# Kernel tuning notes

Hardware: AMD Instinct MI355X
Metric: run time of the kernel (lower is better)

## Reference

```python
import jax, jax.numpy as jnp
import numpy as np

NUM_STEPS = 100
STEP = 2.0 / (NUM_STEPS - 1)          # bin width over [-1, 1]
EPS = 1.0 / NUM_STEPS
TSIZE = NUM_STEPS                      # bin centers t_k = -1 + k*STEP, k=0..99
B, D = 4096, 128
NUM_CLASSES = 100


def setup_inputs() -> dict:
    key = jax.random.key(0)
    k1, k2 = jax.random.split(key)
    embeddings = jax.random.normal(k1, (B, D), dtype=jnp.float32)
    classes = jax.random.randint(k2, (B,), 0, NUM_CLASSES)
    return {"embeddings": embeddings, "classes": classes}


def _histogram_loss(embeddings, classes):
    n = embeddings.shape[0]
    iu, ju = np.triu_indices(n, 1)            # static upper-triangular pair indices
    # cosine similarity of all pairs (outer_cosine_similarity)
    en = embeddings / jnp.linalg.norm(embeddings, axis=1, keepdims=True)
    dists = en @ en.T                          # [B, B]
    s = jnp.clip(dists[iu, ju], -1.0 + 1e-6, 1.0 - 1e-6)   # [P]
    pos = (classes[iu] == classes[ju])         # [P] bool

    # soft triangular-kernel 2-bin scatter (equivalent to indsa/indsb masking):
    # bin j gets (t_j + STEP - s)/STEP, bin j+1 gets (s - t_j)/STEP
    j = jnp.floor((s + 1.0 - 1e-6) / STEP).astype(jnp.int32)   # lower bin index
    t_j = j.astype(s.dtype) * STEP - 1.0
    w_hi = (s - t_j) / STEP                    # weight for bin j+1
    w_lo = (t_j + STEP - s) / STEP             # weight for bin j

    def histogram(mask):
        m = mask.astype(s.dtype)
        size = m.sum()
        h = jnp.zeros((TSIZE,), dtype=s.dtype)
        h = h.at[j].add(w_lo * m).at[j + 1].add(w_hi * m)
        return h / size

    hist_pos = histogram(pos)
    hist_neg = histogram(~pos)
    # tril-masked repeat + sum(0) in the original is exactly a cumulative sum
    hist_pos_cdf = jnp.cumsum(hist_pos)
    return jnp.sum(hist_neg * hist_pos_cdf)


def reference(embeddings, classes):
    return _histogram_loss(embeddings, classes)
```

## Files before the change

### kernel.cpp

```cpp
#include <hip/hip_runtime.h>
#include <hip/hip_bf16.h>
#include <cstddef>

#define BN 4096
#define DD 128
#define NSTEPS 100
#define PTILE 128
#define PLSTR 136
#define GRID_T (BN / PTILE)
#define NOFF 496
#define NBLK 528
#define NREPC 16

typedef __attribute__((ext_vector_type(8))) short bf16x8;
typedef __attribute__((ext_vector_type(4))) float f32x4;

__device__ __forceinline__ void faddf(float* p, float v) { unsafeAtomicAdd(p, v); }

__global__ __launch_bounds__(256) void hl_normalize(const float* __restrict__ emb,
                                                    ushort* __restrict__ out) {
    int w = threadIdx.x >> 6;
    int lane = threadIdx.x & 63;
    int row = (blockIdx.x << 2) + w;
    const float2 v = *(const float2*)(emb + (size_t)row * DD + 2 * lane);
    float ss = v.x * v.x + v.y * v.y;
    #pragma unroll
    for (int off = 32; off > 0; off >>= 1) ss += __shfl_xor(ss, off);
    float inv = 1.0f / sqrtf(ss);
    __hip_bfloat16 b0 = __float2bfloat16(v.x * inv);
    __hip_bfloat16 b1 = __float2bfloat16(v.y * inv);
    ushort2 pk;
    pk.x = *(ushort*)&b0;
    pk.y = *(ushort*)&b1;
    *(ushort2*)(out + (size_t)row * DD + 2 * lane) = pk;
}

__global__ __launch_bounds__(256) void hl_poscls(const ushort* __restrict__ nemb,
                                                 const int* __restrict__ cls,
                                                 float* __restrict__ gPos) {
    const int c = blockIdx.x;
    __shared__ int idx[256];
    __shared__ int scan[256];
    __shared__ ushort As[64 * PLSTR];
    __shared__ ushort Bs[64 * PLSTR];
    __shared__ float hpos[NREPC * 101];
    __shared__ int mTot;
    const int tid = threadIdx.x;

    for (int i = tid; i < NREPC * 101; i += 256) hpos[i] = 0.f;

    const int base = tid * 16;
    int myCnt = 0;
    #pragma unroll
    for (int k = 0; k < 16; ++k) myCnt += (cls[base + k] == c);
    scan[tid] = myCnt;
    __syncthreads();
    for (int s = 1; s < 256; s <<= 1) {
        int v = (tid >= s) ? scan[tid - s] : 0;
        __syncthreads();
        scan[tid] += v;
        __syncthreads();
    }
    int w = scan[tid] - myCnt;
    if (tid == 255) mTot = scan[255] > 256 ? 256 : scan[255];
    #pragma unroll
    for (int k = 0; k < 16; ++k) {
        if (cls[base + k] == c && w < 256) { idx[w] = base + k; ++w; }
    }
    __syncthreads();
    const int m = mTot;
    const int nt = (m + 63) >> 6;

    constexpr float STEPF = 2.0f / 99.0f;
    constexpr float INVSTEP = 49.5f;
    constexpr float CLIPV = 1.0f - 1e-6f;

    const int lane = tid & 63;
    const int wv = tid >> 6;
    const int lr = lane & 15;
    const int kg = lane >> 4;
    const int rep = (lane & 15) * 101;

    for (int si = 0; si < nt; ++si) {
        for (int sj = si; sj < nt; ++sj) {
            __syncthreads();
            #pragma unroll
            for (int it = 0; it < 4; ++it) {
                int q = it * 256 + tid;
                int row = q >> 4;
                int ch = q & 15;
                int ga = si * 64 + row;
                int gb = sj * 64 + row;
                int ra = idx[ga < m ? ga : 0];
                int rb = idx[gb < m ? gb : 0];
                *(float4*)(&As[row * PLSTR + ch * 8]) =
                    *(const float4*)(nemb + (size_t)ra * DD + ch * 8);
                *(float4*)(&Bs[row * PLSTR + ch * 8]) =
                    *(const float4*)(nemb + (size_t)rb * DD + ch * 8);
            }
            __syncthreads();

            f32x4 zero4 = {0.f, 0.f, 0.f, 0.f};
            f32x4 pacc[4] = {zero4, zero4, zero4, zero4};
            #pragma unroll
            for (int ks = 0; ks < 4; ++ks) {
                bf16x8 af = *(const bf16x8*)(&As[(wv * 16 + lr) * PLSTR + ks * 32 + kg * 8]);
                #pragma unroll
                for (int fb = 0; fb < 4; ++fb) {
                    bf16x8 bf = *(const bf16x8*)(&Bs[(fb * 16 + lr) * PLSTR + ks * 32 + kg * 8]);
                    pacc[fb] = __builtin_amdgcn_mfma_f32_16x16x32_bf16(af, bf, pacc[fb], 0, 0, 0);
                }
            }

            #pragma unroll
            for (int fb = 0; fb < 4; ++fb) {
                const int gb = sj * 64 + fb * 16 + lr;
                #pragma unroll
                for (int j = 0; j < 4; ++j) {
                    const int ga = si * 64 + wv * 16 + kg * 4 + j;
                    if (ga < gb && gb < m) {
                        float s = pacc[fb][j];
                        s = fminf(fmaxf(s, -CLIPV), CLIPV);
                        float u = (s + CLIPV) * INVSTEP;
                        int jb = (int)u;
                        if (jb > 98) jb = 98;
                        float t_j = (float)jb * STEPF - 1.0f;
                        float w_hi = (s - t_j) * INVSTEP;
                        float w_lo = 1.0f - w_hi;
                        faddf(&hpos[rep + jb], w_lo);
                        faddf(&hpos[rep + jb + 1], w_hi);
                    }
                }
            }
        }
    }
    __syncthreads();
    if (tid < NSTEPS) {
        float v = 0.f;
        #pragma unroll
        for (int r = 0; r < NREPC; ++r) v += hpos[r * 101 + tid];
        if (v != 0.f) faddf(&gPos[tid], v);
    }
}

__global__ __launch_bounds__(256, 2) void hl_neg(const ushort* __restrict__ nemb,
                                                 const int* __restrict__ cls,
                                                 const float* __restrict__ gPos,
                                                 float* __restrict__ gLoss,
                                                 float* __restrict__ gCnt,
                                                 unsigned int* __restrict__ gDone,
                                                 float* __restrict__ out) {
    int ti, tj;
    {
        int t = blockIdx.x;
        if (t < NOFF) {
            ti = 0;
            int rem = t;
            while (rem >= GRID_T - 1 - ti) { rem -= GRID_T - 1 - ti; ++ti; }
            tj = ti + 1 + rem;
        } else {
            ti = tj = t - NOFF;
        }
    }

    __shared__ ushort As[PTILE * PLSTR];
    __shared__ ushort Bs[PTILE * PLSTR];
    __shared__ float cdfL[NREPC * 101];
    __shared__ float scan[128];
    __shared__ float red[9];
    __shared__ int clsA[PTILE], clsB[PTILE];

    const int tid = threadIdx.x;
    if (tid < PTILE) clsA[tid] = cls[ti * PTILE + tid];
    else             clsB[tid - PTILE] = cls[tj * PTILE + (tid - PTILE)];

    if (tid < 128) scan[tid] = (tid < NSTEPS) ? gPos[tid] : 0.f;
    __syncthreads();
    for (int off = 1; off < 128; off <<= 1) {
        float v = 0.f;
        if (tid < 128 && tid >= off) v = scan[tid - off];
        __syncthreads();
        if (tid < 128) scan[tid] += v;
        __syncthreads();
    }
    if (tid == 0) red[8] = scan[NSTEPS - 1];
    __syncthreads();
    const float invsp = 1.0f / red[8];
    for (int i = tid; i < NREPC * NSTEPS; i += 256) {
        int r = i / NSTEPS, b = i - r * NSTEPS;
        cdfL[r * 101 + b] = scan[b] * invsp;
    }

    #pragma unroll
    for (int it = 0; it < 8; ++it) {
        int idx = it * 256 + tid;
        int row = idx >> 4;
        int cch = idx & 15;
        const float4 va = *(const float4*)(nemb + (size_t)(ti * PTILE + row) * DD + cch * 8);
        const float4 vb = *(const float4*)(nemb + (size_t)(tj * PTILE + row) * DD + cch * 8);
        *(float4*)(&As[row * PLSTR + cch * 8]) = va;
        *(float4*)(&Bs[row * PLSTR + cch * 8]) = vb;
    }
    __syncthreads();

    const int lane = tid & 63;
    const int wid = tid >> 6;
    const int wr = wid >> 1, wc = wid & 1;
    const int lr = lane & 15;
    const int kg = lane >> 4;

    f32x4 zero4 = {0.f, 0.f, 0.f, 0.f};
    f32x4 acc[4][4];
    #pragma unroll
    for (int a = 0; a < 4; ++a)
        #pragma unroll
        for (int b = 0; b < 4; ++b) acc[a][b] = zero4;

    #pragma unroll
    for (int ks = 0; ks < 4; ++ks) {
        bf16x8 af[4], bfr[4];
        #pragma unroll
        for (int f = 0; f < 4; ++f) {
            int arow = wr * 64 + f * 16 + lr;
            af[f] = *(const bf16x8*)(&As[arow * PLSTR + ks * 32 + kg * 8]);
            int brow = wc * 64 + f * 16 + lr;
            bfr[f] = *(const bf16x8*)(&Bs[brow * PLSTR + ks * 32 + kg * 8]);
        }
        #pragma unroll
        for (int fa = 0; fa < 4; ++fa)
            #pragma unroll
            for (int fb = 0; fb < 4; ++fb)
                acc[fa][fb] = __builtin_amdgcn_mfma_f32_16x16x32_bf16(af[fa], bfr[fb], acc[fa][fb], 0, 0, 0);
    }

    constexpr float STEPF = 2.0f / 99.0f;
    constexpr float INVSTEP = 49.5f;
    constexpr float CLIPV = 1.0f - 1e-6f;

    const int li_base = wr * 64 + (kg << 2);
    const int lj_base = wc * 64 + lr;
    const float* crep = &cdfL[(lane & 15) * 101];

    int ca[16];
    #pragma unroll
    for (int fa = 0; fa < 4; ++fa)
        #pragma unroll
        for (int j = 0; j < 4; ++j) ca[fa * 4 + j] = clsA[li_base + fa * 16 + j];

    const bool offdiag = (ti != tj);
    float lacc = 0.f, lcnt = 0.f;

    #pragma unroll
    for (int fb = 0; fb < 4; ++fb) {
        const int lj = lj_base + fb * 16;
        const int cb = clsB[lj];
        #pragma unroll
        for (int fa = 0; fa < 4; ++fa) {
            const int li0 = li_base + fa * 16;
            f32x4 v = acc[fa][fb];
            #pragma unroll
            for (int j = 0; j < 4; ++j) {
                const int li = li0 + j;
                const bool mneg = (offdiag || (li < lj)) && (ca[fa * 4 + j] != cb);
                float s = v[j];
                s = fminf(fmaxf(s, -CLIPV), CLIPV);
                float u = (s + CLIPV) * INVSTEP;
                int jb = (int)u;
                if (jb > 98) jb = 98;
                float t_j = (float)jb * STEPF - 1.0f;
                float w_hi = (s - t_j) * INVSTEP;
                float w_lo = 1.0f - w_hi;
                float c0 = crep[jb];
                float c1 = crep[jb + 1];
                float m = mneg ? 1.0f : 0.0f;
                lacc = fmaf(m, fmaf(w_lo, c0, w_hi * c1), lacc);
                lcnt += m;
            }
        }
    }

    #pragma unroll
    for (int off = 32; off > 0; off >>= 1) {
        lacc += __shfl_xor(lacc, off);
        lcnt += __shfl_xor(lcnt, off);
    }
    if (lane == 0) { red[wid] = lacc; red[4 + wid] = lcnt; }
    __syncthreads();
    if (tid == 0) {
        float L = red[0] + red[1] + red[2] + red[3];
        float C = red[4] + red[5] + red[6] + red[7];
        faddf(&gLoss[blockIdx.x & 31], L);
        faddf(&gCnt[blockIdx.x & 31], C);
        __threadfence();
        unsigned int tk = atomicAdd(gDone, 1u);
        if (tk == NBLK - 1) {
            __threadfence();
            float ls = 0.f, cs = 0.f;
            for (int i = 0; i < 32; ++i) {
                ls += __hip_atomic_load(&gLoss[i], __ATOMIC_RELAXED, __HIP_MEMORY_SCOPE_AGENT);
                cs += __hip_atomic_load(&gCnt[i], __ATOMIC_RELAXED, __HIP_MEMORY_SCOPE_AGENT);
            }
            out[0] = ls / cs;
        }
    }
}

extern "C" void kernel_launch(void* const* d_in, const int* in_sizes, int n_in,
                              void* d_out, int out_size, void* d_ws, size_t ws_size,
                              hipStream_t stream) {
    const float* emb = (const float*)d_in[0];
    const int* classes = (const int*)d_in[1];
    float* out = (float*)d_out;

    ushort* nemb = (ushort*)d_ws;
    float* gPos = (float*)((char*)d_ws + (size_t)BN * DD * sizeof(ushort));
    float* gLoss = gPos + NSTEPS;
    float* gCnt = gLoss + 32;
    unsigned int* gDone = (unsigned int*)(gCnt + 32);

    hipMemsetAsync(gPos, 0, (NSTEPS + 64 + 1) * sizeof(float), stream);

    hl_normalize<<<BN / 4, 256, 0, stream>>>(emb, nemb);
    hl_poscls<<<NSTEPS, 256, 0, stream>>>(nemb, classes, gPos);
    hl_neg<<<NBLK, 256, 0, stream>>>(nemb, classes, gPos, gLoss, gCnt, gDone, out);
}
```

Baseline: 47.03 us.

## Fold memset into normalize, precompute CDF once, use direct-to-LDS swizzled loads

Removes the hipMemsetAsync by zeroing the control block inside the normalize kernel. The last poscls block, chosen with an atomic counter, computes the normalized positive CDF once, so each neg block no longer runs its own prefix scan. The neg kernel packs two diagonal tiles per block, which cuts the grid from 528 to 512 blocks, and diagonal tiles reuse the A tile as B. Tile loads go through global_load_lds into an XOR-swizzled unpadded LDS layout, replacing the padded register-staged copies. The trade-offs are extra serial work in the last poscls block and a longer run for the blocks that handle two diagonal tiles.

```diff
diff --git a/kernel.cpp b/kernel.cpp
--- a/kernel.cpp
+++ b/kernel.cpp
@@ -9,7 +9,7 @@
 #define PLSTR 136
 #define GRID_T (BN / PTILE)
 #define NOFF 496
-#define NBLK 528
+#define NBLK2 512
 #define NREPC 16
 
 typedef __attribute__((ext_vector_type(8))) short bf16x8;
@@ -17,8 +17,12 @@
 
 __device__ __forceinline__ void faddf(float* p, float v) { unsafeAtomicAdd(p, v); }
 
+#define ZERON 166
+
 __global__ __launch_bounds__(256) void hl_normalize(const float* __restrict__ emb,
-                                                    ushort* __restrict__ out) {
+                                                    ushort* __restrict__ out,
+                                                    float* __restrict__ zero_blk) {
+    if (blockIdx.x == 0 && threadIdx.x < ZERON) zero_blk[threadIdx.x] = 0.f;
     int w = threadIdx.x >> 6;
     int lane = threadIdx.x & 63;
     int row = (blockIdx.x << 2) + w;
@@ -37,7 +41,9 @@
 
 __global__ __launch_bounds__(256) void hl_poscls(const ushort* __restrict__ nemb,
                                                  const int* __restrict__ cls,
-                                                 float* __restrict__ gPos) {
+                                                 float* __restrict__ gPos,
+                                                 unsigned int* __restrict__ gDoneP,
+                                                 float* __restrict__ gCdf) {
     const int c = blockIdx.x;
     __shared__ int idx[256];
     __shared__ int scan[256];
@@ -45,6 +51,7 @@
     __shared__ ushort Bs[64 * PLSTR];
     __shared__ float hpos[NREPC * 101];
     __shared__ int mTot;
+    __shared__ int lastFlag;
     const int tid = threadIdx.x;
 
     for (int i = tid; i < NREPC * 101; i += 256) hpos[i] = 0.f;
@@ -141,140 +148,177 @@
         for (int r = 0; r < NREPC; ++r) v += hpos[r * 101 + tid];
         if (v != 0.f) faddf(&gPos[tid], v);
     }
+    __threadfence();
+    if (tid == 0) {
+        unsigned int tk = atomicAdd(gDoneP, 1u);
+        lastFlag = (tk == NSTEPS - 1);
+    }
+    __syncthreads();
+    if (lastFlag) {
+        float v = (tid < NSTEPS)
+            ? __hip_atomic_load(&gPos[tid], __ATOMIC_RELAXED, __HIP_MEMORY_SCOPE_AGENT) : 0.f;
+        if (tid < 128) hpos[tid] = v;
+        __syncthreads();
+        for (int off = 1; off < 128; off <<= 1) {
+            float x = 0.f;
+            if (tid < 128 && tid >= off) x = hpos[tid - off];
+            __syncthreads();
+            if (tid < 128) hpos[tid] += x;
+            __syncthreads();
+        }
+        const float invsp = 1.0f / hpos[NSTEPS - 1];
+        if (tid < NSTEPS) gCdf[tid] = hpos[tid] * invsp;
+    }
 }
 
 __global__ __launch_bounds__(256, 2) void hl_neg(const ushort* __restrict__ nemb,
                                                  const int* __restrict__ cls,
-                                                 const float* __restrict__ gPos,
+                                                 const float* __restrict__ gCdf,
                                                  float* __restrict__ gLoss,
                                                  float* __restrict__ gCnt,
                                                  unsigned int* __restrict__ gDone,
                                                  float* __restrict__ out) {
-    int ti, tj;
-    {
-        int t = blockIdx.x;
-        if (t < NOFF) {
-            ti = 0;
-            int rem = t;
-            while (rem >= GRID_T - 1 - ti) { rem -= GRID_T - 1 - ti; ++ti; }
-            tj = ti + 1 + rem;
-        } else {
-            ti = tj = t - NOFF;
-        }
-    }
-
-    __shared__ ushort As[PTILE * PLSTR];
-    __shared__ ushort Bs[PTILE * PLSTR];
+    __shared__ ushort As[PTILE * 128];
+    __shared__ ushort Bs[PTILE * 128];
     __shared__ float cdfL[NREPC * 101];
-    __shared__ float scan[128];
-    __shared__ float red[9];
+    __shared__ float red[8];
     __shared__ int clsA[PTILE], clsB[PTILE];
 
     const int tid = threadIdx.x;
-    if (tid < PTILE) clsA[tid] = cls[ti * PTILE + tid];
-    else             clsB[tid - PTILE] = cls[tj * PTILE + (tid - PTILE)];
-
-    if (tid < 128) scan[tid] = (tid < NSTEPS) ? gPos[tid] : 0.f;
-    __syncthreads();
-    for (int off = 1; off < 128; off <<= 1) {
-        float v = 0.f;
-        if (tid < 128 && tid >= off) v = scan[tid - off];
-        __syncthreads();
-        if (tid < 128) scan[tid] += v;
-        __syncthreads();
-    }
-    if (tid == 0) red[8] = scan[NSTEPS - 1];
-    __syncthreads();
-    const float invsp = 1.0f / red[8];
-    for (int i = tid; i < NREPC * NSTEPS; i += 256) {
-        int r = i / NSTEPS, b = i - r * NSTEPS;
-        cdfL[r * 101 + b] = scan[b] * invsp;
-    }
-
-    #pragma unroll
-    for (int it = 0; it < 8; ++it) {
-        int idx = it * 256 + tid;
-        int row = idx >> 4;
-        int cch = idx & 15;
-        const float4 va = *(const float4*)(nemb + (size_t)(ti * PTILE + row) * DD + cch * 8);
-        const float4 vb = *(const float4*)(nemb + (size_t)(tj * PTILE + row) * DD + cch * 8);
-        *(float4*)(&As[row * PLSTR + cch * 8]) = va;
-        *(float4*)(&Bs[row * PLSTR + cch * 8]) = vb;
-    }
-    __syncthreads();
-
     const int lane = tid & 63;
     const int wid = tid >> 6;
     const int wr = wid >> 1, wc = wid & 1;
     const int lr = lane & 15;
     const int kg = lane >> 4;
 
-    f32x4 zero4 = {0.f, 0.f, 0.f, 0.f};
-    f32x4 acc[4][4];
-    #pragma unroll
-    for (int a = 0; a < 4; ++a)
-        #pragma unroll
-        for (int b = 0; b < 4; ++b) acc[a][b] = zero4;
-
-    #pragma unroll
-    for (int ks = 0; ks < 4; ++ks) {
-        bf16x8 af[4], bfr[4];
-        #pragma unroll
-        for (int f = 0; f < 4; ++f) {
-            int arow = wr * 64 + f * 16 + lr;
-            af[f] = *(const bf16x8*)(&As[arow * PLSTR + ks * 32 + kg * 8]);
-            int brow = wc * 64 + f * 16 + lr;
-            bfr[f] = *(const bf16x8*)(&Bs[brow * PLSTR + ks * 32 + kg * 8]);
-        }
-        #pragma unroll
-        for (int fa = 0; fa < 4; ++fa)
-            #pragma unroll
-            for (int fb = 0; fb < 4; ++fb)
-                acc[fa][fb] = __builtin_amdgcn_mfma_f32_16x16x32_bf16(af[fa], bfr[fb], acc[fa][fb], 0, 0, 0);
+    int ti0, tj0, ti1 = 0, nu = 1;
+    {
+        int t = blockIdx.x;
+        if (t < NOFF) {
+            int ti = 0, rem = t;
+            while (rem >= GRID_T - 1 - ti) { rem -= GRID_T - 1 - ti; ++ti; }
+            ti0 = ti; tj0 = ti + 1 + rem;
+        } else {
+            int d = (t - NOFF) * 2;
+            ti0 = tj0 = d; ti1 = d + 1; nu = 2;
+        }
+    }
+
+    for (int i = tid; i < NREPC * NSTEPS; i += 256) {
+        int r = i / NSTEPS, b = i - r * NSTEPS;
+        cdfL[r * 101 + b] = gCdf[b];
     }
 
     constexpr float STEPF = 2.0f / 99.0f;
     constexpr float INVSTEP = 49.5f;
     constexpr float CLIPV = 1.0f - 1e-6f;
-
+    const float* crep = &cdfL[(lane & 15) * 101];
     const int li_base = wr * 64 + (kg << 2);
     const int lj_base = wc * 64 + lr;
-    const float* crep = &cdfL[(lane & 15) * 101];
-
-    int ca[16];
-    #pragma unroll
-    for (int fa = 0; fa < 4; ++fa)
-        #pragma unroll
-        for (int j = 0; j < 4; ++j) ca[fa * 4 + j] = clsA[li_base + fa * 16 + j];
-
-    const bool offdiag = (ti != tj);
+
     float lacc = 0.f, lcnt = 0.f;
-
-    #pragma unroll
-    for (int fb = 0; fb < 4; ++fb) {
-        const int lj = lj_base + fb * 16;
-        const int cb = clsB[lj];
-        #pragma unroll
-        for (int fa = 0; fa < 4; ++fa) {
-            const int li0 = li_base + fa * 16;
-            f32x4 v = acc[fa][fb];
-            #pragma unroll
-            for (int j = 0; j < 4; ++j) {
-                const int li = li0 + j;
-                const bool mneg = (offdiag || (li < lj)) && (ca[fa * 4 + j] != cb);
-                float s = v[j];
-                s = fminf(fmaxf(s, -CLIPV), CLIPV);
-                float u = (s + CLIPV) * INVSTEP;
-                int jb = (int)u;
-                if (jb > 98) jb = 98;
-                float t_j = (float)jb * STEPF - 1.0f;
-                float w_hi = (s - t_j) * INVSTEP;
-                float w_lo = 1.0f - w_hi;
-                float c0 = crep[jb];
-                float c1 = crep[jb + 1];
-                float m = mneg ? 1.0f : 0.0f;
-                lacc = fmaf(m, fmaf(w_lo, c0, w_hi * c1), lacc);
-                lcnt += m;
+    const int rloc = lane >> 4;
+    const int pch = lane & 15;
+
+    for (int u = 0; u < nu; ++u) {
+        const int ti = u ? ti1 : ti0;
+        const int tj = u ? ti1 : tj0;
+        const bool diag = (ti == tj);
+
+        __syncthreads();
+        if (tid < PTILE) clsA[tid] = cls[ti * PTILE + tid];
+        else             clsB[tid - PTILE] = cls[tj * PTILE + (tid - PTILE)];
+
+        {
+            const ushort* Ag = nemb + (size_t)(ti * PTILE) * DD;
+            const ushort* Bg = nemb + (size_t)(tj * PTILE) * DD;
+            #pragma unroll
+            for (int t = 0; t < 8; ++t) {
+                int row = wid * 32 + t * 4 + rloc;
+                int lch = pch ^ (row & 7);
+                const ushort* ga = Ag + (size_t)row * DD + lch * 8;
+                ushort* la = &As[(wid * 32 + t * 4) * 128];
+                __builtin_amdgcn_global_load_lds(
+                    (const __attribute__((address_space(1))) void*)ga,
+                    (__attribute__((address_space(3))) void*)la, 16, 0, 0);
+            }
+            if (!diag) {
+                #pragma unroll
+                for (int t = 0; t < 8; ++t) {
+                    int row = wid * 32 + t * 4 + rloc;
+                    int lch = pch ^ (row & 7);
+                    const ushort* gb = Bg + (size_t)row * DD + lch * 8;
+                    ushort* lb = &Bs[(wid * 32 + t * 4) * 128];
+                    __builtin_amdgcn_global_load_lds(
+                        (const __attribute__((address_space(1))) void*)gb,
+                        (__attribute__((address_space(3))) void*)lb, 16, 0, 0);
+                }
+            }
+        }
+        __syncthreads();
+
+        const ushort* Bsel = diag ? As : Bs;
+        const int* clsBsel = diag ? clsA : clsB;
+
+        f32x4 zero4 = {0.f, 0.f, 0.f, 0.f};
+        f32x4 acc[4][4];
+        #pragma unroll
+        for (int a = 0; a < 4; ++a)
+            #pragma unroll
+            for (int b = 0; b < 4; ++b) acc[a][b] = zero4;
+
+        #pragma unroll
+        for (int ks = 0; ks < 4; ++ks) {
+            bf16x8 af[4], bfr[4];
+            #pragma unroll
+            for (int f = 0; f < 4; ++f) {
+                int arow = wr * 64 + f * 16 + lr;
+                int pca = ((ks << 2) | kg) ^ (arow & 7);
+                af[f] = *(const bf16x8*)(&As[arow * 128 + pca * 8]);
+                int brow = wc * 64 + f * 16 + lr;
+                int pcb = ((ks << 2) | kg) ^ (brow & 7);
+                bfr[f] = *(const bf16x8*)(&Bsel[brow * 128 + pcb * 8]);
+            }
+            #pragma unroll
+            for (int fa = 0; fa < 4; ++fa)
+                #pragma unroll
+                for (int fb = 0; fb < 4; ++fb)
+                    acc[fa][fb] = __builtin_amdgcn_mfma_f32_16x16x32_bf16(af[fa], bfr[fb], acc[fa][fb], 0, 0, 0);
+        }
+
+        int ca[16];
+        #pragma unroll
+        for (int fa = 0; fa < 4; ++fa)
+            #pragma unroll
+            for (int j = 0; j < 4; ++j) ca[fa * 4 + j] = clsA[li_base + fa * 16 + j];
+
+        const bool offdiag = !diag;
+        #pragma unroll
+        for (int fb = 0; fb < 4; ++fb) {
+            const int lj = lj_base + fb * 16;
+            const int cb = clsBsel[lj];
+            #pragma unroll
+            for (int fa = 0; fa < 4; ++fa) {
+                const int li0 = li_base + fa * 16;
+                f32x4 v = acc[fa][fb];
+                #pragma unroll
+                for (int j = 0; j < 4; ++j) {
+                    const int li = li0 + j;
+                    const bool mneg = (offdiag || (li < lj)) && (ca[fa * 4 + j] != cb);
+                    float s = v[j];
+                    s = fminf(fmaxf(s, -CLIPV), CLIPV);
+                    float uu = (s + CLIPV) * INVSTEP;
+                    int jb = (int)uu;
+                    if (jb > 98) jb = 98;
+                    float t_j = (float)jb * STEPF - 1.0f;
+                    float w_hi = (s - t_j) * INVSTEP;
+                    float w_lo = 1.0f - w_hi;
+                    float c0 = crep[jb];
+                    float c1 = crep[jb + 1];
+                    float mm = mneg ? 1.0f : 0.0f;
+                    lacc = fmaf(mm, fmaf(w_lo, c0, w_hi * c1), lacc);
+                    lcnt += mm;
+                }
             }
         }
     }
@@ -293,7 +337,7 @@
         faddf(&gCnt[blockIdx.x & 31], C);
         __threadfence();
         unsigned int tk = atomicAdd(gDone, 1u);
-        if (tk == NBLK - 1) {
+        if (tk == NBLK2 - 1) {
             __threadfence();
             float ls = 0.f, cs = 0.f;
             for (int i = 0; i < 32; ++i) {
@@ -313,14 +357,15 @@
     float* out = (float*)d_out;
 
     ushort* nemb = (ushort*)d_ws;
-    float* gPos = (float*)((char*)d_ws + (size_t)BN * DD * sizeof(ushort));
+    float* ctl = (float*)((char*)d_ws + (size_t)BN * DD * sizeof(ushort));
+    float* gPos = ctl;
     float* gLoss = gPos + NSTEPS;
     float* gCnt = gLoss + 32;
     unsigned int* gDone = (unsigned int*)(gCnt + 32);
-
-    hipMemsetAsync(gPos, 0, (NSTEPS + 64 + 1) * sizeof(float), stream);
-
-    hl_normalize<<<BN / 4, 256, 0, stream>>>(emb, nemb);
-    hl_poscls<<<NSTEPS, 256, 0, stream>>>(nemb, classes, gPos);
-    hl_neg<<<NBLK, 256, 0, stream>>>(nemb, classes, gPos, gLoss, gCnt, gDone, out);
+    unsigned int* gDoneP = gDone + 1;
+    float* gCdf = (float*)(gDoneP + 1);
+
+    hl_normalize<<<BN / 4, 256, 0, stream>>>(emb, nemb, ctl);
+    hl_poscls<<<NSTEPS, 256, 0, stream>>>(nemb, classes, gPos, gDoneP, gCdf);
+    hl_neg<<<NBLK2, 256, 0, stream>>>(nemb, classes, gCdf, gLoss, gCnt, gDone, out);
 }
```

After: 46.34 us. About the same (-1.5%).
